# Performance work log

Measured on AMD Instinct MI355X. Metric: run time of the kernel, lower is better.

Reference implementation:

```python
import jax, jax.numpy as jnp
import numpy as np

PAD = -2.0 ** 16 + 1.0  # tf code uses -2**16+1 as masked logit
ITERATIONS = 3


def squash(x):
    # x: [..., out_units]
    n = jnp.sum(jnp.square(x), axis=-1, keepdims=True)
    return (n / (1.0 + n) / jnp.sqrt(n + 1e-9)) * x


def setup_inputs() -> dict:
    key = jax.random.key(0)
    k1, k2, k3, k4 = jax.random.split(key, 4)
    B, L, DIN, DOUT, K = 4096, 200, 64, 64, 8
    return {
        "low_capsule": jax.random.normal(k1, (B, L, DIN), dtype=jnp.float32),
        "seq_len": jax.random.randint(k2, (B, 1), 1, L + 1, dtype=jnp.int32),
        "B_matrix": jax.random.normal(k3, (1, K, L), dtype=jnp.float32),
        "S_matrix": jax.random.normal(k4, (DIN, DOUT), dtype=jnp.float32),
    }


def reference(low_capsule, seq_len, B_matrix, S_matrix):
    # low_capsule: [B, L, Din]; seq_len: [B, 1]; B_matrix: [1, K, L]; S_matrix: [Din, Dout]
    L = B_matrix.shape[2]
    # tf.sequence_mask(tile(seq_len,[1,K]), L) -> [B, K, L]; K axis broadcasts.
    mask = jnp.arange(L)[None, None, :] < seq_len[:, :, None]  # [B, 1, L]
    # low_capsule_new is identical every iteration; compute once.
    low_new = jnp.einsum('bli,io->blo', low_capsule, S_matrix)  # [B, L, Dout]
    Bc = B_matrix  # routing logits, updated (stateful assign_add in tf)
    high = None
    for _ in range(ITERATIONS):
        logits = jnp.where(mask, Bc, PAD)  # [B, K, L]
        W = jax.nn.softmax(logits, axis=-1)
        high = squash(jnp.einsum('bkl,blo->bko', W, low_new))  # [B, K, Dout]
        # B_delta = sum_b high @ low_new^T, keepdims on batch
        Bc = Bc + jnp.einsum('bko,blo->kl', high, low_new)[None]  # [1, K, L]
    return high
```

## Files before the change

### kernel.cpp

```cpp
#include <hip/hip_runtime.h>
#include <math.h>


#define B_SZ  4096
#define L_SZ  200
#define DINK  64
#define DOUTK 64
#define K_SZ  8

__global__ __launch_bounds__(256) void k_init(const float* __restrict__ Bm,
                                              const float* __restrict__ S,
                                              float* __restrict__ Bc,
                                              float* __restrict__ St) {
    int i = blockIdx.x * 256 + threadIdx.x;
    if (i < K_SZ * L_SZ) Bc[i] = Bm[i];
    int j = i - K_SZ * L_SZ;
    if (j >= 0 && j < DINK * DOUTK) {
        int o = j >> 6, ii = j & 63;
        St[j] = S[ii * DOUTK + o];
    }
}

template<int WRITE_OUT>
__global__ __launch_bounds__(256) void k_route(const float* __restrict__ lc_g,
                                               const int* __restrict__ seq_len,
                                               const float* __restrict__ S_g,
                                               const float* __restrict__ St_g,
                                               const float* __restrict__ Bc,
                                               float* __restrict__ partial,
                                               float* __restrict__ out) {
    __shared__ float W_s[K_SZ][L_SZ];
    __shared__ float hp_s[K_SZ][DINK];
    __shared__ float ovl[4 * K_SZ * DINK];
    float (*hp_part)[K_SZ][DINK] = (float (*)[K_SZ][DINK])ovl;
    float (*hx_s)[DINK] = (float (*)[DINK])(ovl);
    float (*hs_s)[DINK] = (float (*)[DINK])(ovl + K_SZ * DINK);

    int t = threadIdx.x;
    int b = blockIdx.x;
    long lbase = (long)b * (L_SZ * DINK);
    const float* lcb = lc_g + lbase;
    int sl = seq_len[b];
    int k = t >> 5, g = t & 31;
    int w = t >> 6, c = t & 63;

    const float* bk = Bc + k * L_SZ;
    float m = -3.4e38f;
    for (int l = g; l < sl; l += 32) m = fmaxf(m, bk[l]);
    #pragma unroll
    for (int s = 16; s; s >>= 1) m = fmaxf(m, __shfl_xor(m, s, 32));
    float sum = 0.f;
    for (int l = g; l < sl; l += 32) {
        float e = __expf(bk[l] - m);
        sum += e;
        W_s[k][l] = e;
    }
    #pragma unroll
    for (int s = 16; s; s >>= 1) sum += __shfl_xor(sum, s, 32);
    float rinv = 1.0f / sum;
    __syncthreads();

    {
        float acc[K_SZ];
        #pragma unroll
        for (int kk = 0; kk < K_SZ; ++kk) acc[kk] = 0.f;
        for (int l = 4 * w; l < sl; l += 16) {
            if (l + 4 <= sl) {
                float v0 = lcb[(l + 0) * DINK + c];
                float v1 = lcb[(l + 1) * DINK + c];
                float v2 = lcb[(l + 2) * DINK + c];
                float v3 = lcb[(l + 3) * DINK + c];
                #pragma unroll
                for (int kk = 0; kk < K_SZ; ++kk) {
                    float4 w4 = *(const float4*)&W_s[kk][l];
                    acc[kk] += w4.x * v0 + w4.y * v1 + w4.z * v2 + w4.w * v3;
                }
            } else {
                for (int u = l; u < sl; ++u) {
                    float v = lcb[u * DINK + c];
                    #pragma unroll
                    for (int kk = 0; kk < K_SZ; ++kk) acc[kk] += W_s[kk][u] * v;
                }
            }
        }
        #pragma unroll
        for (int kk = 0; kk < K_SZ; ++kk) hp_part[w][kk][c] = acc[kk];
    }
    __syncthreads();

    {
        float2 r = make_float2(0.f, 0.f);
        #pragma unroll
        for (int cc = 0; cc < 4; ++cc) {
            float2 p = *(const float2*)&hp_part[cc][k][2 * g];
            r.x += p.x; r.y += p.y;
        }
        *(float2*)&hp_s[k][2 * g] = make_float2(r.x * rinv, r.y * rinv);
    }
    __syncthreads();

    {
        float h0 = 0.f, h1 = 0.f;
        const float* sp = S_g + 2 * g;
        #pragma unroll 8
        for (int i = 0; i < DINK; ++i) {
            float p = hp_s[k][i];
            float2 sv = *(const float2*)(sp + i * DOUTK);
            h0 += p * sv.x; h1 += p * sv.y;
        }
        float nn = h0 * h0 + h1 * h1;
        #pragma unroll
        for (int s = 16; s; s >>= 1) nn += __shfl_xor(nn, s, 32);
        float sc = nn / ((1.0f + nn) * sqrtf(nn + 1e-9f));
        h0 *= sc; h1 *= sc;
        if (WRITE_OUT) {
            float2* ob2 = (float2*)(out + (long)b * (K_SZ * DOUTK) + k * DOUTK);
            ob2[g] = make_float2(h0, h1);
            return;
        }
        *(float2*)&hx_s[k][2 * g] = make_float2(h0, h1);
    }

    {
        float s0 = 0.f, s1 = 0.f;
        const float* stp = St_g + 2 * g;
        #pragma unroll 8
        for (int o = 0; o < DOUTK; ++o) {
            float hv = hx_s[k][o];
            float2 sv = *(const float2*)(stp + o * DINK);
            s0 += hv * sv.x; s1 += hv * sv.y;
        }
        *(float2*)&hs_s[k][2 * g] = make_float2(s0, s1);
    }
    __syncthreads();

    if (t < L_SZ) {
        const float4* row4 = (const float4*)(lcb + (long)t * DINK);
        float* pb = partial + (long)b * (K_SZ * L_SZ);
        float acc[K_SZ] = {};
        #pragma unroll
        for (int i4 = 0; i4 < 16; ++i4) {
            float4 v = row4[i4];
            #pragma unroll
            for (int kk = 0; kk < K_SZ; ++kk) {
                float4 h = *(const float4*)&hs_s[kk][i4 * 4];
                acc[kk] += v.x * h.x + v.y * h.y + v.z * h.z + v.w * h.w;
            }
        }
        #pragma unroll
        for (int kk = 0; kk < K_SZ; ++kk)
            pb[kk * L_SZ + t] = acc[kk];
    }
}

__global__ __launch_bounds__(256) void k_reduceA(const float* __restrict__ partial,
                                                 float* __restrict__ partial2) {
    __shared__ float red[256];
    int x = blockIdx.x % 50;
    int y = blockIdx.x / 50;
    int t = threadIdx.x;
    int i = x * 32 + (t & 31);
    int sub = t >> 5;
    float s = 0.f;
    for (int p = y * 256 + sub; p < (y + 1) * 256; p += 8)
        s += partial[(long)p * (K_SZ * L_SZ) + i];
    red[t] = s;
    __syncthreads();
    for (int step = 4; step >= 1; step >>= 1) {
        if (sub < step) red[t] += red[t + step * 32];
        __syncthreads();
    }
    if (sub == 0) partial2[y * (K_SZ * L_SZ) + i] = red[t];
}

__global__ __launch_bounds__(256) void k_reduceB(const float* __restrict__ partial2,
                                                 float* __restrict__ Bc) {
    int i = blockIdx.x * 256 + threadIdx.x;
    if (i < K_SZ * L_SZ) {
        float s = 0.f;
        #pragma unroll
        for (int y = 0; y < 16; ++y) s += partial2[y * (K_SZ * L_SZ) + i];
        Bc[i] += s;
    }
}

extern "C" void kernel_launch(void* const* d_in, const int* in_sizes, int n_in,
                              void* d_out, int out_size, void* d_ws, size_t ws_size,
                              hipStream_t stream) {
    const float* lc = (const float*)d_in[0];
    const int*   sl = (const int*)d_in[1];
    const float* Bm = (const float*)d_in[2];
    const float* S  = (const float*)d_in[3];
    float* out = (float*)d_out;
    float* ws  = (float*)d_ws;

    float* Bc      = ws;
    float* St      = ws + 1600;
    float* partial = St + 4096;
    float* p2      = out;

    k_init<<<23, 256, 0, stream>>>(Bm, S, Bc, St);

    k_route<0><<<B_SZ, 256, 0, stream>>>(lc, sl, S, St, Bc, partial, out);
    k_reduceA <<<800, 256, 0, stream>>>(partial, p2);
    k_reduceB <<<7, 256, 0, stream>>>(p2, Bc);
    k_route<0><<<B_SZ, 256, 0, stream>>>(lc, sl, S, St, Bc, partial, out);
    k_reduceA <<<800, 256, 0, stream>>>(partial, p2);
    k_reduceB <<<7, 256, 0, stream>>>(p2, Bc);
    k_route<1><<<B_SZ, 256, 0, stream>>>(lc, sl, S, St, Bc, partial, out);
}
```

Baseline: 287.4 us.

## Split softmax into separate kernel and map one wavefront per batch in routing

```diff
diff --git a/kernel.cpp b/kernel.cpp
--- a/kernel.cpp
+++ b/kernel.cpp
@@ -4,9 +4,12 @@
 
 #define B_SZ  4096
 #define L_SZ  200
-#define DINK  64
-#define DOUTK 64
+#define DK    64
 #define K_SZ  8
+
+__device__ __forceinline__ float rl(float x, int i) {
+    return __int_as_float(__builtin_amdgcn_readlane(__float_as_int(x), i));
+}
 
 __global__ __launch_bounds__(256) void k_init(const float* __restrict__ Bm,
                                               const float* __restrict__ S,
@@ -15,34 +18,19 @@
     int i = blockIdx.x * 256 + threadIdx.x;
     if (i < K_SZ * L_SZ) Bc[i] = Bm[i];
     int j = i - K_SZ * L_SZ;
-    if (j >= 0 && j < DINK * DOUTK) {
+    if (j >= 0 && j < DK * DK) {
         int o = j >> 6, ii = j & 63;
-        St[j] = S[ii * DOUTK + o];
-    }
-}
-
-template<int WRITE_OUT>
-__global__ __launch_bounds__(256) void k_route(const float* __restrict__ lc_g,
-                                               const int* __restrict__ seq_len,
-                                               const float* __restrict__ S_g,
-                                               const float* __restrict__ St_g,
-                                               const float* __restrict__ Bc,
-                                               float* __restrict__ partial,
-                                               float* __restrict__ out) {
+        St[j] = S[ii * DK + o];
+    }
+}
+
+__global__ __launch_bounds__(256) void k_soft(const int* __restrict__ seq_len,
+                                              const float* __restrict__ Bc,
+                                              float* __restrict__ Wt_g) {
     __shared__ float W_s[K_SZ][L_SZ];
-    __shared__ float hp_s[K_SZ][DINK];
-    __shared__ float ovl[4 * K_SZ * DINK];
-    float (*hp_part)[K_SZ][DINK] = (float (*)[K_SZ][DINK])ovl;
-    float (*hx_s)[DINK] = (float (*)[DINK])(ovl);
-    float (*hs_s)[DINK] = (float (*)[DINK])(ovl + K_SZ * DINK);
-
-    int t = threadIdx.x;
-    int b = blockIdx.x;
-    long lbase = (long)b * (L_SZ * DINK);
-    const float* lcb = lc_g + lbase;
+    int t = threadIdx.x, b = blockIdx.x;
+    int k = t >> 5, g = t & 31;
     int sl = seq_len[b];
-    int k = t >> 5, g = t & 31;
-    int w = t >> 6, c = t & 63;
 
     const float* bk = Bc + k * L_SZ;
     float m = -3.4e38f;
@@ -50,106 +38,123 @@
     #pragma unroll
     for (int s = 16; s; s >>= 1) m = fmaxf(m, __shfl_xor(m, s, 32));
     float sum = 0.f;
-    for (int l = g; l < sl; l += 32) {
-        float e = __expf(bk[l] - m);
+    for (int l = g; l < L_SZ; l += 32) {
+        float e = (l < sl) ? __expf(bk[l] - m) : 0.f;
         sum += e;
         W_s[k][l] = e;
     }
     #pragma unroll
     for (int s = 16; s; s >>= 1) sum += __shfl_xor(sum, s, 32);
     float rinv = 1.0f / sum;
+    for (int l = g; l < L_SZ; l += 32) W_s[k][l] *= rinv;
     __syncthreads();
 
-    {
-        float acc[K_SZ];
-        #pragma unroll
-        for (int kk = 0; kk < K_SZ; ++kk) acc[kk] = 0.f;
-        for (int l = 4 * w; l < sl; l += 16) {
-            if (l + 4 <= sl) {
-                float v0 = lcb[(l + 0) * DINK + c];
-                float v1 = lcb[(l + 1) * DINK + c];
-                float v2 = lcb[(l + 2) * DINK + c];
-                float v3 = lcb[(l + 3) * DINK + c];
-                #pragma unroll
-                for (int kk = 0; kk < K_SZ; ++kk) {
-                    float4 w4 = *(const float4*)&W_s[kk][l];
-                    acc[kk] += w4.x * v0 + w4.y * v1 + w4.z * v2 + w4.w * v3;
-                }
-            } else {
-                for (int u = l; u < sl; ++u) {
-                    float v = lcb[u * DINK + c];
-                    #pragma unroll
-                    for (int kk = 0; kk < K_SZ; ++kk) acc[kk] += W_s[kk][u] * v;
-                }
+    float* dst = Wt_g + (long)b * (K_SZ * L_SZ);
+    for (int j = t; j < K_SZ * L_SZ; j += 256)
+        dst[j] = W_s[j & 7][j >> 3];
+}
+
+template<int WRITE_OUT>
+__global__ __launch_bounds__(256, 4) void k_route3(const float* __restrict__ lc_g,
+                                                   const float* __restrict__ Wt_g,
+                                                   const float* __restrict__ S_g,
+                                                   const float* __restrict__ St_g,
+                                                   float* __restrict__ partial,
+                                                   float* __restrict__ out) {
+    int t = threadIdx.x;
+    int lam = t & 63;
+    int wv = __builtin_amdgcn_readfirstlane(t >> 6);
+    int b = blockIdx.x * 4 + wv;
+    const float* __restrict__ lcb = lc_g + (long)b * (L_SZ * DK);
+    const float* __restrict__ wt  = Wt_g + (long)b * (K_SZ * L_SZ);
+
+    float acc[K_SZ] = {0.f, 0.f, 0.f, 0.f, 0.f, 0.f, 0.f, 0.f};
+    {
+        const float* lp = lcb + lam;
+        #pragma unroll 4
+        for (int l = 0; l < L_SZ; ++l) {
+            float v = lp[l * DK];
+            float4 wa = *(const float4*)(wt + l * K_SZ);
+            float4 wb = *(const float4*)(wt + l * K_SZ + 4);
+            acc[0] = fmaf(wa.x, v, acc[0]);
+            acc[1] = fmaf(wa.y, v, acc[1]);
+            acc[2] = fmaf(wa.z, v, acc[2]);
+            acc[3] = fmaf(wa.w, v, acc[3]);
+            acc[4] = fmaf(wb.x, v, acc[4]);
+            acc[5] = fmaf(wb.y, v, acc[5]);
+            acc[6] = fmaf(wb.z, v, acc[6]);
+            acc[7] = fmaf(wb.w, v, acc[7]);
+        }
+    }
+
+    float h[K_SZ] = {0.f, 0.f, 0.f, 0.f, 0.f, 0.f, 0.f, 0.f};
+    {
+        const float* sp = S_g + lam;
+        for (int i = 0; i < DK; ++i) {
+            float v = sp[i * DK];
+            #pragma unroll
+            for (int k = 0; k < K_SZ; ++k)
+                h[k] = fmaf(rl(acc[k], i), v, h[k]);
+        }
+    }
+
+    #pragma unroll
+    for (int k = 0; k < K_SZ; ++k) {
+        float nn = h[k] * h[k];
+        #pragma unroll
+        for (int s = 1; s < 64; s <<= 1) nn += __shfl_xor(nn, s, 64);
+        float sc = nn / ((1.0f + nn) * sqrtf(nn + 1e-9f));
+        h[k] *= sc;
+    }
+
+    if (WRITE_OUT) {
+        float* ob = out + (long)b * (K_SZ * DK) + lam;
+        #pragma unroll
+        for (int k = 0; k < K_SZ; ++k) ob[k * DK] = h[k];
+        return;
+    }
+
+    float hs[K_SZ] = {0.f, 0.f, 0.f, 0.f, 0.f, 0.f, 0.f, 0.f};
+    {
+        const float* sp = St_g + lam;
+        for (int o = 0; o < DK; ++o) {
+            float v = sp[o * DK];
+            #pragma unroll
+            for (int k = 0; k < K_SZ; ++k)
+                hs[k] = fmaf(rl(h[k], o), v, hs[k]);
+        }
+    }
+
+    {
+        int live3 = (lam < 8);
+        int r3 = live3 ? (192 + lam) : 0;
+        const float4* p0 = (const float4*)(lcb + (long)lam * DK);
+        const float4* p1 = (const float4*)(lcb + (long)(64 + lam) * DK);
+        const float4* p2 = (const float4*)(lcb + (long)(128 + lam) * DK);
+        const float4* p3 = (const float4*)(lcb + (long)r3 * DK);
+        float a0[K_SZ] = {}, a1[K_SZ] = {}, a2[K_SZ] = {}, a3[K_SZ] = {};
+        for (int i4 = 0; i4 < 16; ++i4) {
+            float4 v0 = p0[i4], v1 = p1[i4], v2 = p2[i4], v3 = p3[i4];
+            #pragma unroll
+            for (int k = 0; k < K_SZ; ++k) {
+                float s0 = rl(hs[k], 4 * i4 + 0);
+                float s1 = rl(hs[k], 4 * i4 + 1);
+                float s2 = rl(hs[k], 4 * i4 + 2);
+                float s3 = rl(hs[k], 4 * i4 + 3);
+                a0[k] = fmaf(s0, v0.x, fmaf(s1, v0.y, fmaf(s2, v0.z, fmaf(s3, v0.w, a0[k]))));
+                a1[k] = fmaf(s0, v1.x, fmaf(s1, v1.y, fmaf(s2, v1.z, fmaf(s3, v1.w, a1[k]))));
+                a2[k] = fmaf(s0, v2.x, fmaf(s1, v2.y, fmaf(s2, v2.z, fmaf(s3, v2.w, a2[k]))));
+                a3[k] = fmaf(s0, v3.x, fmaf(s1, v3.y, fmaf(s2, v3.z, fmaf(s3, v3.w, a3[k]))));
             }
         }
-        #pragma unroll
-        for (int kk = 0; kk < K_SZ; ++kk) hp_part[w][kk][c] = acc[kk];
-    }
-    __syncthreads();
-
-    {
-        float2 r = make_float2(0.f, 0.f);
-        #pragma unroll
-        for (int cc = 0; cc < 4; ++cc) {
-            float2 p = *(const float2*)&hp_part[cc][k][2 * g];
-            r.x += p.x; r.y += p.y;
-        }
-        *(float2*)&hp_s[k][2 * g] = make_float2(r.x * rinv, r.y * rinv);
-    }
-    __syncthreads();
-
-    {
-        float h0 = 0.f, h1 = 0.f;
-        const float* sp = S_g + 2 * g;
-        #pragma unroll 8
-        for (int i = 0; i < DINK; ++i) {
-            float p = hp_s[k][i];
-            float2 sv = *(const float2*)(sp + i * DOUTK);
-            h0 += p * sv.x; h1 += p * sv.y;
-        }
-        float nn = h0 * h0 + h1 * h1;
-        #pragma unroll
-        for (int s = 16; s; s >>= 1) nn += __shfl_xor(nn, s, 32);
-        float sc = nn / ((1.0f + nn) * sqrtf(nn + 1e-9f));
-        h0 *= sc; h1 *= sc;
-        if (WRITE_OUT) {
-            float2* ob2 = (float2*)(out + (long)b * (K_SZ * DOUTK) + k * DOUTK);
-            ob2[g] = make_float2(h0, h1);
-            return;
-        }
-        *(float2*)&hx_s[k][2 * g] = make_float2(h0, h1);
-    }
-
-    {
-        float s0 = 0.f, s1 = 0.f;
-        const float* stp = St_g + 2 * g;
-        #pragma unroll 8
-        for (int o = 0; o < DOUTK; ++o) {
-            float hv = hx_s[k][o];
-            float2 sv = *(const float2*)(stp + o * DINK);
-            s0 += hv * sv.x; s1 += hv * sv.y;
-        }
-        *(float2*)&hs_s[k][2 * g] = make_float2(s0, s1);
-    }
-    __syncthreads();
-
-    if (t < L_SZ) {
-        const float4* row4 = (const float4*)(lcb + (long)t * DINK);
         float* pb = partial + (long)b * (K_SZ * L_SZ);
-        float acc[K_SZ] = {};
-        #pragma unroll
-        for (int i4 = 0; i4 < 16; ++i4) {
-            float4 v = row4[i4];
-            #pragma unroll
-            for (int kk = 0; kk < K_SZ; ++kk) {
-                float4 h = *(const float4*)&hs_s[kk][i4 * 4];
-                acc[kk] += v.x * h.x + v.y * h.y + v.z * h.z + v.w * h.w;
-            }
-        }
-        #pragma unroll
-        for (int kk = 0; kk < K_SZ; ++kk)
-            pb[kk * L_SZ + t] = acc[kk];
+        #pragma unroll
+        for (int k = 0; k < K_SZ; ++k) {
+            pb[k * L_SZ + lam]       = a0[k];
+            pb[k * L_SZ + 64 + lam]  = a1[k];
+            pb[k * L_SZ + 128 + lam] = a2[k];
+            if (live3) pb[k * L_SZ + 192 + lam] = a3[k];
+        }
     }
 }
 
@@ -195,17 +200,23 @@
     float* ws  = (float*)d_ws;
 
     float* Bc      = ws;
-    float* St      = ws + 1600;
-    float* partial = St + 4096;
+    float* St      = Bc + 1600;
+    float* Wt      = St + 4096;
+    float* partial = Wt + (long)B_SZ * K_SZ * L_SZ;
     float* p2      = out;
 
     k_init<<<23, 256, 0, stream>>>(Bm, S, Bc, St);
 
-    k_route<0><<<B_SZ, 256, 0, stream>>>(lc, sl, S, St, Bc, partial, out);
-    k_reduceA <<<800, 256, 0, stream>>>(partial, p2);
-    k_reduceB <<<7, 256, 0, stream>>>(p2, Bc);
-    k_route<0><<<B_SZ, 256, 0, stream>>>(lc, sl, S, St, Bc, partial, out);
-    k_reduceA <<<800, 256, 0, stream>>>(partial, p2);
-    k_reduceB <<<7, 256, 0, stream>>>(p2, Bc);
-    k_route<1><<<B_SZ, 256, 0, stream>>>(lc, sl, S, St, Bc, partial, out);
-}
+    k_soft     <<<B_SZ, 256, 0, stream>>>(sl, Bc, Wt);
+    k_route3<0><<<B_SZ / 4, 256, 0, stream>>>(lc, Wt, S, St, partial, out);
+    k_reduceA  <<<800, 256, 0, stream>>>(partial, p2);
+    k_reduceB  <<<7, 256, 0, stream>>>(p2, Bc);
+
+    k_soft     <<<B_SZ, 256, 0, stream>>>(sl, Bc, Wt);
+    k_route3<0><<<B_SZ / 4, 256, 0, stream>>>(lc, Wt, S, St, partial, out);
+    k_reduceA  <<<800, 256, 0, stream>>>(partial, p2);
+    k_reduceB  <<<7, 256, 0, stream>>>(p2, Bc);
+
+    k_soft     <<<B_SZ, 256, 0, stream>>>(sl, Bc, Wt);
+    k_route3<1><<<B_SZ / 4, 256, 0, stream>>>(lc, Wt, S, St, partial, out);
+}
```

Measured after the change: 583.7 us. 2.03x slower.

## Precompute softmax weights per sequence length and use readlane broadcasts in routing

Applied to the files above, without the earlier changes.

```diff
diff --git a/kernel.cpp b/kernel.cpp
--- a/kernel.cpp
+++ b/kernel.cpp
@@ -4,9 +4,12 @@
 
 #define B_SZ  4096
 #define L_SZ  200
-#define DINK  64
-#define DOUTK 64
+#define DK    64
 #define K_SZ  8
+
+__device__ __forceinline__ float rl(float x, int i) {
+    return __int_as_float(__builtin_amdgcn_readlane(__float_as_int(x), i));
+}
 
 __global__ __launch_bounds__(256) void k_init(const float* __restrict__ Bm,
                                               const float* __restrict__ S,
@@ -15,141 +18,152 @@
     int i = blockIdx.x * 256 + threadIdx.x;
     if (i < K_SZ * L_SZ) Bc[i] = Bm[i];
     int j = i - K_SZ * L_SZ;
-    if (j >= 0 && j < DINK * DOUTK) {
+    if (j >= 0 && j < DK * DK) {
         int o = j >> 6, ii = j & 63;
-        St[j] = S[ii * DOUTK + o];
-    }
+        St[j] = S[ii * DK + o];
+    }
+}
+
+__global__ __launch_bounds__(256) void k_soft(const float* __restrict__ Bc,
+                                              float* __restrict__ Wt_g) {
+    __shared__ float W_s[K_SZ][L_SZ];
+    int t = threadIdx.x;
+    int s = blockIdx.x + 1;
+    int k = t >> 5, g = t & 31;
+
+    const float* bk = Bc + k * L_SZ;
+    float m = -3.4e38f;
+    for (int l = g; l < s; l += 32) m = fmaxf(m, bk[l]);
+    #pragma unroll
+    for (int st = 16; st; st >>= 1) m = fmaxf(m, __shfl_xor(m, st, 32));
+    float sum = 0.f;
+    for (int l = g; l < L_SZ; l += 32) {
+        float e = (l < s) ? __expf(bk[l] - m) : 0.f;
+        sum += e;
+        W_s[k][l] = e;
+    }
+    #pragma unroll
+    for (int st = 16; st; st >>= 1) sum += __shfl_xor(sum, st, 32);
+    float rinv = 1.0f / sum;
+    for (int l = g; l < L_SZ; l += 32) W_s[k][l] *= rinv;
+    __syncthreads();
+
+    float* dst = Wt_g + (long)(s - 1) * (K_SZ * L_SZ);
+    for (int j = t; j < K_SZ * L_SZ; j += 256)
+        dst[j] = W_s[j & 7][j >> 3];
 }
 
 template<int WRITE_OUT>
-__global__ __launch_bounds__(256) void k_route(const float* __restrict__ lc_g,
-                                               const int* __restrict__ seq_len,
-                                               const float* __restrict__ S_g,
-                                               const float* __restrict__ St_g,
-                                               const float* __restrict__ Bc,
-                                               float* __restrict__ partial,
-                                               float* __restrict__ out) {
-    __shared__ float W_s[K_SZ][L_SZ];
-    __shared__ float hp_s[K_SZ][DINK];
-    __shared__ float ovl[4 * K_SZ * DINK];
-    float (*hp_part)[K_SZ][DINK] = (float (*)[K_SZ][DINK])ovl;
-    float (*hx_s)[DINK] = (float (*)[DINK])(ovl);
-    float (*hs_s)[DINK] = (float (*)[DINK])(ovl + K_SZ * DINK);
-
+__global__ __launch_bounds__(256, 8) void k_route4(const float* __restrict__ lc_g,
+                                                   const int* __restrict__ seq_len,
+                                                   const float* __restrict__ Wt_g,
+                                                   const float* __restrict__ S_g,
+                                                   const float* __restrict__ St_g,
+                                                   float* __restrict__ partial,
+                                                   float* __restrict__ out) {
+    __shared__ float hp_part[4][K_SZ][DK];
+    __shared__ float hp_s[K_SZ][DK];
+    __shared__ float hs_s[K_SZ][DK];
     int t = threadIdx.x;
     int b = blockIdx.x;
-    long lbase = (long)b * (L_SZ * DINK);
-    const float* lcb = lc_g + lbase;
+    const float* __restrict__ lcb = lc_g + (long)b * (L_SZ * DK);
+    int k = t >> 5, g = t & 31;
+    int lam = t & 63;
+    int w = __builtin_amdgcn_readfirstlane(t >> 6);
+
     int sl = seq_len[b];
-    int k = t >> 5, g = t & 31;
-    int w = t >> 6, c = t & 63;
-
-    const float* bk = Bc + k * L_SZ;
-    float m = -3.4e38f;
-    for (int l = g; l < sl; l += 32) m = fmaxf(m, bk[l]);
-    #pragma unroll
-    for (int s = 16; s; s >>= 1) m = fmaxf(m, __shfl_xor(m, s, 32));
-    float sum = 0.f;
-    for (int l = g; l < sl; l += 32) {
-        float e = __expf(bk[l] - m);
-        sum += e;
-        W_s[k][l] = e;
-    }
-    #pragma unroll
-    for (int s = 16; s; s >>= 1) sum += __shfl_xor(sum, s, 32);
-    float rinv = 1.0f / sum;
-    __syncthreads();
-
-    {
-        float acc[K_SZ];
-        #pragma unroll
-        for (int kk = 0; kk < K_SZ; ++kk) acc[kk] = 0.f;
-        for (int l = 4 * w; l < sl; l += 16) {
-            if (l + 4 <= sl) {
-                float v0 = lcb[(l + 0) * DINK + c];
-                float v1 = lcb[(l + 1) * DINK + c];
-                float v2 = lcb[(l + 2) * DINK + c];
-                float v3 = lcb[(l + 3) * DINK + c];
-                #pragma unroll
-                for (int kk = 0; kk < K_SZ; ++kk) {
-                    float4 w4 = *(const float4*)&W_s[kk][l];
-                    acc[kk] += w4.x * v0 + w4.y * v1 + w4.z * v2 + w4.w * v3;
-                }
-            } else {
-                for (int u = l; u < sl; ++u) {
-                    float v = lcb[u * DINK + c];
-                    #pragma unroll
-                    for (int kk = 0; kk < K_SZ; ++kk) acc[kk] += W_s[kk][u] * v;
-                }
-            }
-        }
-        #pragma unroll
-        for (int kk = 0; kk < K_SZ; ++kk) hp_part[w][kk][c] = acc[kk];
-    }
-    __syncthreads();
-
-    {
+    const float* __restrict__ wbase = Wt_g + (long)(sl - 1) * (K_SZ * L_SZ);
+
+    float acc[K_SZ] = {};
+    {
+        const float* lp = lcb + lam;
+        #pragma unroll 2
+        for (int j = 0; j < 50; ++j) {
+            int l = w + 4 * j;
+            float v = lp[l * DK];
+            const float* wr = wbase + l * K_SZ;
+            acc[0] = fmaf(wr[0], v, acc[0]);
+            acc[1] = fmaf(wr[1], v, acc[1]);
+            acc[2] = fmaf(wr[2], v, acc[2]);
+            acc[3] = fmaf(wr[3], v, acc[3]);
+            acc[4] = fmaf(wr[4], v, acc[4]);
+            acc[5] = fmaf(wr[5], v, acc[5]);
+            acc[6] = fmaf(wr[6], v, acc[6]);
+            acc[7] = fmaf(wr[7], v, acc[7]);
+        }
+        #pragma unroll
+        for (int kk = 0; kk < K_SZ; ++kk) hp_part[w][kk][lam] = acc[kk];
+    }
+    __syncthreads();
+
+    {
+        int kk = t >> 5, ii = (t & 31) * 2;
         float2 r = make_float2(0.f, 0.f);
         #pragma unroll
-        for (int cc = 0; cc < 4; ++cc) {
-            float2 p = *(const float2*)&hp_part[cc][k][2 * g];
+        for (int ww = 0; ww < 4; ++ww) {
+            float2 p = *(const float2*)&hp_part[ww][kk][ii];
             r.x += p.x; r.y += p.y;
         }
-        *(float2*)&hp_s[k][2 * g] = make_float2(r.x * rinv, r.y * rinv);
-    }
-    __syncthreads();
-
-    {
-        float h0 = 0.f, h1 = 0.f;
+        *(float2*)&hp_s[kk][ii] = r;
+    }
+    __syncthreads();
+
+    float h0 = 0.f, h1 = 0.f;
+    {
         const float* sp = S_g + 2 * g;
         #pragma unroll 8
-        for (int i = 0; i < DINK; ++i) {
-            float p = hp_s[k][i];
-            float2 sv = *(const float2*)(sp + i * DOUTK);
-            h0 += p * sv.x; h1 += p * sv.y;
+        for (int i = 0; i < DK; ++i) {
+            float pv = hp_s[k][i];
+            float2 sv = *(const float2*)(sp + i * DK);
+            h0 = fmaf(pv, sv.x, h0); h1 = fmaf(pv, sv.y, h1);
         }
         float nn = h0 * h0 + h1 * h1;
         #pragma unroll
-        for (int s = 16; s; s >>= 1) nn += __shfl_xor(nn, s, 32);
+        for (int st = 16; st; st >>= 1) nn += __shfl_xor(nn, st, 32);
         float sc = nn / ((1.0f + nn) * sqrtf(nn + 1e-9f));
         h0 *= sc; h1 *= sc;
-        if (WRITE_OUT) {
-            float2* ob2 = (float2*)(out + (long)b * (K_SZ * DOUTK) + k * DOUTK);
-            ob2[g] = make_float2(h0, h1);
-            return;
-        }
-        *(float2*)&hx_s[k][2 * g] = make_float2(h0, h1);
-    }
+    }
+    if (WRITE_OUT) {
+        float2* ob2 = (float2*)(out + (long)b * (K_SZ * DK) + k * DK);
+        ob2[g] = make_float2(h0, h1);
+        return;
+    }
+    *(float2*)&hp_s[k][2 * g] = make_float2(h0, h1);
 
     {
         float s0 = 0.f, s1 = 0.f;
         const float* stp = St_g + 2 * g;
         #pragma unroll 8
-        for (int o = 0; o < DOUTK; ++o) {
-            float hv = hx_s[k][o];
-            float2 sv = *(const float2*)(stp + o * DINK);
-            s0 += hv * sv.x; s1 += hv * sv.y;
+        for (int o = 0; o < DK; ++o) {
+            float hv = hp_s[k][o];
+            float2 sv = *(const float2*)(stp + o * DK);
+            s0 = fmaf(hv, sv.x, s0); s1 = fmaf(hv, sv.y, s1);
         }
         *(float2*)&hs_s[k][2 * g] = make_float2(s0, s1);
     }
     __syncthreads();
 
+    float hsr[K_SZ];
+    #pragma unroll
+    for (int kk = 0; kk < K_SZ; ++kk) hsr[kk] = hs_s[kk][lam];
     if (t < L_SZ) {
-        const float4* row4 = (const float4*)(lcb + (long)t * DINK);
-        float* pb = partial + (long)b * (K_SZ * L_SZ);
-        float acc[K_SZ] = {};
+        const float4* row4 = (const float4*)(lcb + (long)t * DK);
+        float a[K_SZ] = {};
         #pragma unroll
         for (int i4 = 0; i4 < 16; ++i4) {
             float4 v = row4[i4];
             #pragma unroll
             for (int kk = 0; kk < K_SZ; ++kk) {
-                float4 h = *(const float4*)&hs_s[kk][i4 * 4];
-                acc[kk] += v.x * h.x + v.y * h.y + v.z * h.z + v.w * h.w;
+                a[kk] = fmaf(rl(hsr[kk], 4 * i4 + 0), v.x,
+                        fmaf(rl(hsr[kk], 4 * i4 + 1), v.y,
+                        fmaf(rl(hsr[kk], 4 * i4 + 2), v.z,
+                        fmaf(rl(hsr[kk], 4 * i4 + 3), v.w, a[kk]))));
             }
         }
+        float* pb = partial + (long)b * (K_SZ * L_SZ);
         #pragma unroll
         for (int kk = 0; kk < K_SZ; ++kk)
-            pb[kk * L_SZ + t] = acc[kk];
+            pb[kk * L_SZ + t] = a[kk];
     }
 }
 
@@ -195,17 +209,23 @@
     float* ws  = (float*)d_ws;
 
     float* Bc      = ws;
-    float* St      = ws + 1600;
-    float* partial = St + 4096;
+    float* St      = Bc + 1600;
+    float* Wt      = St + 4096;
+    float* partial = Wt + 200 * (K_SZ * L_SZ);
     float* p2      = out;
 
     k_init<<<23, 256, 0, stream>>>(Bm, S, Bc, St);
 
-    k_route<0><<<B_SZ, 256, 0, stream>>>(lc, sl, S, St, Bc, partial, out);
-    k_reduceA <<<800, 256, 0, stream>>>(partial, p2);
-    k_reduceB <<<7, 256, 0, stream>>>(p2, Bc);
-    k_route<0><<<B_SZ, 256, 0, stream>>>(lc, sl, S, St, Bc, partial, out);
-    k_reduceA <<<800, 256, 0, stream>>>(partial, p2);
-    k_reduceB <<<7, 256, 0, stream>>>(p2, Bc);
-    k_route<1><<<B_SZ, 256, 0, stream>>>(lc, sl, S, St, Bc, partial, out);
-}
+    k_soft     <<<200, 256, 0, stream>>>(Bc, Wt);
+    k_route4<0><<<B_SZ, 256, 0, stream>>>(lc, sl, Wt, S, St, partial, out);
+    k_reduceA  <<<800, 256, 0, stream>>>(partial, p2);
+    k_reduceB  <<<7, 256, 0, stream>>>(p2, Bc);
+
+    k_soft     <<<200, 256, 0, stream>>>(Bc, Wt);
+    k_route4<0><<<B_SZ, 256, 0, stream>>>(lc, sl, Wt, S, St, partial, out);
+    k_reduceA  <<<800, 256, 0, stream>>>(partial, p2);
+    k_reduceB  <<<7, 256, 0, stream>>>(p2, Bc);
+
+    k_soft     <<<200, 256, 0, stream>>>(Bc, Wt);
+    k_route4<1><<<B_SZ, 256, 0, stream>>>(lc, sl, Wt, S, St, partial, out);
+}
```

After: 328.9 us. +14.4%, slower.
